# Kernel tuning notes

Measured on AMD Instinct MI355X. Metric: run time of the kernel, lower is better.

The kernel has to match this reference:

```python
import jax, jax.numpy as jnp
import numpy as np

B, D_IN, D_H = 16384, 512, 1024


def _glorot(key, out_d, in_d):
    lim = 1.0 / np.sqrt(in_d)
    return jax.random.uniform(key, (out_d, in_d), minval=-lim, maxval=lim, dtype=jnp.float32)


def setup_inputs() -> dict:
    key = jax.random.key(0)
    ks = jax.random.split(key, 16)
    inp = {
        "x_t": jax.random.normal(ks[0], (B, D_IN), dtype=jnp.float32),
        "delta_t": jax.random.uniform(ks[1], (B, 1), dtype=jnp.float32),
        "h_prev": jax.random.normal(ks[2], (B, D_H), dtype=jnp.float32),
        # torch nn.Linear weights are [out, in]; y = x @ W.T
        "W_sh": _glorot(ks[3], D_H, D_H),
        "W_sx": _glorot(ks[4], D_H, D_IN),
        "W_st": _glorot(ks[5], D_H, 1),
        "b_s": jnp.zeros((D_H,), jnp.float32),
        "WTh": _glorot(ks[6], D_H, D_H),
        "WTx": _glorot(ks[7], D_H, D_IN),
        "WTs": _glorot(ks[8], D_H, D_H),
        "b_T": jnp.zeros((D_H,), jnp.float32),
        "W_rh": _glorot(ks[9], D_H, D_H),
        "W_rx": _glorot(ks[10], D_H, D_IN),
        "b_r": jnp.zeros((D_H,), jnp.float32),
        "W_zh": _glorot(ks[11], D_H, D_H),
        "W_zx": _glorot(ks[12], D_H, D_IN),
        "b_z": jnp.zeros((D_H,), jnp.float32),
        "W_h": _glorot(ks[13], D_H, D_H),
        "W_x": _glorot(ks[14], D_H, D_IN),
        "b": jnp.zeros((D_H,), jnp.float32),
    }
    return inp


def reference(x_t, delta_t, h_prev,
              W_sh, W_sx, W_st, b_s,
              WTh, WTx, WTs, b_T,
              W_rh, W_rx, b_r,
              W_zh, W_zx, b_z,
              W_h, W_x, b):
    lin = lambda x, W: x @ W.T  # nn.Linear(bias=False)
    s_t = jnp.tanh(lin(h_prev, W_sh) + lin(x_t, W_sx) + lin(delta_t, W_st) + b_s)
    T_t = jax.nn.sigmoid(lin(h_prev, WTh) + lin(x_t, WTx) + lin(s_t, WTs) + b_T)
    r_t = jax.nn.sigmoid(lin(h_prev, W_rh) + lin(x_t, W_rx) + b_r)
    z_t = jax.nn.sigmoid(lin(h_prev, W_zh) + lin(x_t, W_zx) + b_z)
    h_tilde = jnp.tanh(lin(r_t * h_prev, W_h) + lin(x_t, W_x) + b)
    h_t = (1.0 - z_t) * (T_t * h_prev) + z_t * h_tilde
    return h_t
```

## Files before the change

### kernel.cpp

```cpp
#include <hip/hip_runtime.h>
#include <stdint.h>

#define AS1 __attribute__((address_space(1)))
#define AS3 __attribute__((address_space(3)))

typedef unsigned short US;
typedef __bf16 bf16x8 __attribute__((ext_vector_type(8)));
typedef float f32x4 __attribute__((ext_vector_type(4)));

static constexpr int Bsz = 16384;
static constexpr int DIN = 512;
static constexpr int DH  = 1024;
static constexpr int LDA = 2560;
static constexpr int LDR = 1536;

__device__ __forceinline__ US f2bf(float f) {
  unsigned u = __float_as_uint(f);
  u += 0x7fffu + ((u >> 16) & 1u);
  return (US)(u >> 16);
}
__device__ __forceinline__ float bf2f(US u) { return __uint_as_float(((unsigned)u) << 16); }
__device__ __forceinline__ float sigm(float x) { return 1.f / (1.f + __expf(-x)); }
__device__ __forceinline__ float tanh_f(float x) { return 1.f - 2.f / (1.f + __expf(2.f * x)); }

__global__ void pack_A(const float* __restrict__ h, const float* __restrict__ x,
                       US* __restrict__ Ab, US* __restrict__ RHx) {
  const int total = Bsz * 384;
  for (int idx = blockIdx.x * blockDim.x + threadIdx.x; idx < total;
       idx += gridDim.x * blockDim.x) {
    int row = idx / 384;
    int c = (idx - row * 384) * 4;
    const float* src = (c < DH) ? (h + (size_t)row * DH + c)
                                : (x + (size_t)row * DIN + (c - DH));
    float4 v = *(const float4*)src;
    ushort4 o;
    o.x = f2bf(v.x); o.y = f2bf(v.y); o.z = f2bf(v.z); o.w = f2bf(v.w);
    *(ushort4*)(Ab + (size_t)row * LDA + c) = o;
    if (c >= DH) *(ushort4*)(RHx + (size_t)row * LDR + c) = o;
  }
}

struct WSlot { const float* src; US* dst; int n4; int ksh; int ld; int co; };
struct WBatch { WSlot s[11]; };
__global__ void conv_w(WBatch b) {
  WSlot sl = b.s[blockIdx.y];
  const int mask = (1 << sl.ksh) - 1;
  for (int i = blockIdx.x * blockDim.x + threadIdx.x; i < sl.n4;
       i += gridDim.x * blockDim.x) {
    float4 v = *(const float4*)(sl.src + (size_t)i * 4);
    ushort4 o;
    o.x = f2bf(v.x); o.y = f2bf(v.y); o.z = f2bf(v.z); o.w = f2bf(v.w);
    int r = i >> sl.ksh;
    int cc = (i & mask) * 4;
    *(ushort4*)(sl.dst + (size_t)r * sl.ld + sl.co + cc) = o;
  }
}

template <int EPI>
__global__ __launch_bounds__(512, 2) void gemm8(
    const US* __restrict__ A, int lda,
    const US* __restrict__ W, int ldw, int nt,
    const float* __restrict__ bias,
    const void* aux0, const void* aux1, const void* aux2,
    void* outp, int ldo) {
  __shared__ __align__(16) US As[2][256 * 64];
  __shared__ __align__(16) US Bs[2][256 * 64];

  const int tid  = threadIdx.x;
  const int lane = tid & 63;
  const int w    = tid >> 6;
  const int wr   = w >> 2;
  const int wc   = w & 3;
  const int quad = lane >> 4, l15 = lane & 15;
  const int sw8  = l15 & 7;
  const int lrow = lane >> 3;
  const int scc  = (lane & 7) ^ (lrow & 7);

  const int p = blockIdx.x;
  const int c = p & 7, q = p >> 3;
  const int nIdx = q & 3, mIdx = c * 8 + (q >> 2);
  const int mBase = mIdx * 256, nBase = nIdx * 256;

  f32x4 acc[8][4];
#pragma unroll
  for (int i = 0; i < 8; i++)
#pragma unroll
    for (int j = 0; j < 4; j++) acc[i][j] = f32x4{0.f, 0.f, 0.f, 0.f};

#define STAGE_A(d, hh, tt)                                                       \
  { const US* g = A + (size_t)(mBase + (hh)*128 + w * 8 + lrow) * lda +          \
                  (tt) * 64 + scc * 8;                                           \
    __builtin_amdgcn_global_load_lds((AS1 const void*)g,                         \
        (AS3 void*)&As[d][((hh)*128 + w * 8) * 64], 16, 0, 0);                   \
    __builtin_amdgcn_global_load_lds((AS1 const void*)(g + (size_t)64 * lda),    \
        (AS3 void*)&As[d][((hh)*128 + 64 + w * 8) * 64], 16, 0, 0); }
#define STAGE_B(d, hh, tt)                                                       \
  { const US* g = W + (size_t)(nBase + (hh)*128 + w * 8 + lrow) * ldw +          \
                  (tt) * 64 + scc * 8;                                           \
    __builtin_amdgcn_global_load_lds((AS1 const void*)g,                         \
        (AS3 void*)&Bs[d][((hh)*128 + w * 8) * 64], 16, 0, 0);                   \
    __builtin_amdgcn_global_load_lds((AS1 const void*)(g + (size_t)64 * ldw),    \
        (AS3 void*)&Bs[d][((hh)*128 + 64 + w * 8) * 64], 16, 0, 0); }

#define READ_A(mh)                                                               \
  _Pragma("unroll")                                                              \
  for (int i = 0; i < 4; ++i)                                                    \
    _Pragma("unroll")                                                            \
    for (int ks = 0; ks < 2; ++ks)                                               \
      af[i][ks] = *(const bf16x8*)&As[cur][(wr * 128 + (mh)*64 + i * 16 + l15)   \
                                          * 64 + (((ks * 4 + quad) ^ sw8) * 8)];
#define READ_B(BSET, nh)                                                         \
  _Pragma("unroll")                                                              \
  for (int j = 0; j < 2; ++j)                                                    \
    _Pragma("unroll")                                                            \
    for (int ks = 0; ks < 2; ++ks)                                               \
      BSET[j][ks] = *(const bf16x8*)&Bs[cur][(wc * 64 + (nh)*32 + j * 16 + l15)  \
                                            * 64 + (((ks * 4 + quad) ^ sw8) * 8)];
#define MFMA_Q(mh, BSET, nh)                                                     \
  _Pragma("unroll")                                                              \
  for (int ks = 0; ks < 2; ++ks)                                                 \
    _Pragma("unroll")                                                            \
    for (int i = 0; i < 4; ++i)                                                  \
      _Pragma("unroll")                                                          \
      for (int j = 0; j < 2; ++j)                                                \
        acc[(mh)*4 + i][(nh)*2 + j] = __builtin_amdgcn_mfma_f32_16x16x32_bf16(   \
            af[i][ks], BSET[j][ks], acc[(mh)*4 + i][(nh)*2 + j], 0, 0, 0);

  STAGE_A(0, 0, 0); STAGE_A(0, 1, 0); STAGE_B(0, 0, 0); STAGE_B(0, 1, 0);
  if (nt > 1) { STAGE_B(1, 0, 1); STAGE_B(1, 1, 1); }
  if (nt > 1) __builtin_amdgcn_s_waitcnt(0x0f74);
  else        __builtin_amdgcn_s_waitcnt(0x0f70);
  __builtin_amdgcn_s_barrier();
  __builtin_amdgcn_sched_barrier(0);

  bf16x8 af[4][2], b0[2][2], b1[2][2];
  int cur = 0;

  for (int t = 0; t < nt; ++t, cur ^= 1) {
    const int nxt = cur ^ 1;
    READ_A(0);
    READ_B(b0, 0);
    if (t + 1 < nt) STAGE_A(nxt, 0, t + 1);
    __builtin_amdgcn_s_barrier();
    __builtin_amdgcn_s_setprio(1);
    MFMA_Q(0, b0, 0);
    __builtin_amdgcn_s_setprio(0);
    __builtin_amdgcn_s_barrier();
    READ_B(b1, 1);
    if (t + 1 < nt) STAGE_A(nxt, 1, t + 1);
    __builtin_amdgcn_s_barrier();
    __builtin_amdgcn_s_setprio(1);
    MFMA_Q(0, b1, 1);
    __builtin_amdgcn_s_setprio(0);
    __builtin_amdgcn_s_barrier();
    READ_A(1);
    if (t + 2 < nt) STAGE_B(cur, 0, t + 2);
    __builtin_amdgcn_s_barrier();
    __builtin_amdgcn_s_setprio(1);
    MFMA_Q(1, b0, 0);
    __builtin_amdgcn_s_setprio(0);
    __builtin_amdgcn_s_barrier();
    if (t + 2 < nt) STAGE_B(cur, 1, t + 2);
    __builtin_amdgcn_s_barrier();
    __builtin_amdgcn_s_setprio(1);
    MFMA_Q(1, b1, 1);
    __builtin_amdgcn_s_setprio(0);
    if (t + 1 < nt) {
      if (t + 2 < nt) __builtin_amdgcn_s_waitcnt(0x0f74);
      else            __builtin_amdgcn_s_waitcnt(0x0f70);
      __builtin_amdgcn_s_barrier();
      __builtin_amdgcn_sched_barrier(0);
    }
  }
#undef STAGE_A
#undef STAGE_B
#undef READ_A
#undef READ_B
#undef MFMA_Q

#pragma unroll
  for (int im = 0; im < 8; ++im) {
#pragma unroll
    for (int jn = 0; jn < 4; ++jn) {
      const int col = nBase + wc * 64 + jn * 16 + l15;
      const float bv = bias[col];
#pragma unroll
      for (int r = 0; r < 4; ++r) {
        const int row = mBase + wr * 128 + im * 16 + quad * 4 + r;
        float v = acc[im][jn][r] + bv;
        if constexpr (EPI == 0) {
          const float* delta = (const float*)aux0;
          const float* wst   = (const float*)aux1;
          v += delta[row] * wst[col];
          ((US*)outp)[(size_t)row * ldo + col] = f2bf(tanh_f(v));
        } else if constexpr (EPI == 1) {
          const float* hp = (const float*)aux0;
          float rr = sigm(v);
          ((US*)outp)[(size_t)row * ldo + col] =
              f2bf(rr * hp[(size_t)row * DH + col]);
        } else if constexpr (EPI == 2) {
          ((US*)outp)[(size_t)row * ldo + col] = f2bf(sigm(v));
        } else if constexpr (EPI == 3) {
          ((US*)outp)[(size_t)row * ldo + col] = f2bf(tanh_f(v));
        } else {
          const float* hp = (const float*)aux0;
          const US* Zp = (const US*)aux1;
          const US* Hp = (const US*)aux2;
          float T = sigm(v);
          size_t o = (size_t)row * DH + col;
          float z = bf2f(Zp[o]), ht = bf2f(Hp[(size_t)row * LDR + col]);
          float h = hp[o];
          ((float*)outp)[(size_t)row * ldo + col] = (1.f - z) * (T * h) + z * ht;
        }
      }
    }
  }
}

extern "C" void kernel_launch(void* const* d_in, const int* in_sizes, int n_in,
                              void* d_out, int out_size, void* d_ws, size_t ws_size,
                              hipStream_t stream) {
  const float* x_t   = (const float*)d_in[0];
  const float* delta = (const float*)d_in[1];
  const float* h_prev= (const float*)d_in[2];
  const float* W_sh  = (const float*)d_in[3];
  const float* W_sx  = (const float*)d_in[4];
  const float* W_st  = (const float*)d_in[5];
  const float* b_s   = (const float*)d_in[6];
  const float* WTh   = (const float*)d_in[7];
  const float* WTx   = (const float*)d_in[8];
  const float* WTs   = (const float*)d_in[9];
  const float* b_T   = (const float*)d_in[10];
  const float* W_rh  = (const float*)d_in[11];
  const float* W_rx  = (const float*)d_in[12];
  const float* b_r   = (const float*)d_in[13];
  const float* W_zh  = (const float*)d_in[14];
  const float* W_zx  = (const float*)d_in[15];
  const float* b_z   = (const float*)d_in[16];
  const float* W_h   = (const float*)d_in[17];
  const float* W_x   = (const float*)d_in[18];
  const float* b_    = (const float*)d_in[19];
  float* out = (float*)d_out;

  char* ws = (char*)d_ws;
  US* Ab = (US*)ws;                         size_t off = (size_t)Bsz * LDA * 2;
  US* RH = (US*)(ws + off);                 off += (size_t)Bsz * LDR * 2;
  US* Zb = (US*)(ws + off);                 off += (size_t)Bsz * DH * 2;
  US* bWs = (US*)(ws + off); off += (size_t)DH * 1536 * 2;
  US* bWr = (US*)(ws + off); off += (size_t)DH * 1536 * 2;
  US* bWz = (US*)(ws + off); off += (size_t)DH * 1536 * 2;
  US* bWT = (US*)(ws + off); off += (size_t)DH * 2560 * 2;
  US* bWh = (US*)(ws + off); off += (size_t)DH * 1536 * 2;

  pack_A<<<dim3(8192), 256, 0, stream>>>(h_prev, x_t, Ab, RH);
  WBatch wb;
  const int n4h = DH * DH / 4, n4x = DH * DIN / 4;
  wb.s[0]  = {W_sh, bWs, n4h, 8, 1536, 0};
  wb.s[1]  = {W_sx, bWs, n4x, 7, 1536, 1024};
  wb.s[2]  = {W_rh, bWr, n4h, 8, 1536, 0};
  wb.s[3]  = {W_rx, bWr, n4x, 7, 1536, 1024};
  wb.s[4]  = {W_zh, bWz, n4h, 8, 1536, 0};
  wb.s[5]  = {W_zx, bWz, n4x, 7, 1536, 1024};
  wb.s[6]  = {WTh,  bWT, n4h, 8, 2560, 0};
  wb.s[7]  = {WTx,  bWT, n4x, 7, 2560, 1024};
  wb.s[8]  = {WTs,  bWT, n4h, 8, 2560, 1536};
  wb.s[9]  = {W_h,  bWh, n4h, 8, 1536, 0};
  wb.s[10] = {W_x,  bWh, n4x, 7, 1536, 1024};
  conv_w<<<dim3(512, 11), 256, 0, stream>>>(wb);

  const dim3 grid(256);

  gemm8<0><<<grid, 512, 0, stream>>>(Ab, LDA, bWs, 1536, 24, b_s,
                                     delta, W_st, nullptr, (void*)(Ab + 1536), LDA);
  gemm8<1><<<grid, 512, 0, stream>>>(Ab, LDA, bWr, 1536, 24, b_r,
                                     h_prev, nullptr, nullptr, (void*)RH, LDR);
  gemm8<2><<<grid, 512, 0, stream>>>(Ab, LDA, bWz, 1536, 24, b_z,
                                     nullptr, nullptr, nullptr, (void*)Zb, DH);
  gemm8<3><<<grid, 512, 0, stream>>>(RH, LDR, bWh, 1536, 24, b_,
                                     nullptr, nullptr, nullptr, (void*)RH, LDR);
  gemm8<4><<<grid, 512, 0, stream>>>(Ab, LDA, bWT, 2560, 40, b_T,
                                     h_prev, Zb, RH, (void*)out, DH);
}
```

Baseline: 577.1 us.

## Fuse s/r/z gate GEMMs into one launch and deepen LDS prefetch pipeline

Concatenates the s, r and z weight matrices into one 3072-row weight buffer and computes all three gates in a single GEMM launch with 768 blocks, picking the epilogue per N-block group. The main loop now prefetches both A and B two k-tiles ahead, issues LDS reads as inline ds_read_b128 with explicit lgkmcnt waits and sched barriers, and waits on vmcnt(8). h_tilde is written to a separate buffer instead of overwriting RH. The aim is fewer launches, a larger grid to fill the GPU, and better overlap of global loads with MFMA, at the cost of extra workspace and hand-managed waits that are fragile.

```diff
diff --git a/kernel.cpp b/kernel.cpp
--- a/kernel.cpp
+++ b/kernel.cpp
@@ -7,6 +7,7 @@
 typedef unsigned short US;
 typedef __bf16 bf16x8 __attribute__((ext_vector_type(8)));
 typedef float f32x4 __attribute__((ext_vector_type(4)));
+typedef int intx4 __attribute__((ext_vector_type(4)));
 
 static constexpr int Bsz = 16384;
 static constexpr int DIN = 512;
@@ -22,6 +23,16 @@
 __device__ __forceinline__ float bf2f(US u) { return __uint_as_float(((unsigned)u) << 16); }
 __device__ __forceinline__ float sigm(float x) { return 1.f / (1.f + __expf(-x)); }
 __device__ __forceinline__ float tanh_f(float x) { return 1.f - 2.f / (1.f + __expf(2.f * x)); }
+
+__device__ __forceinline__ intx4 dsr128(unsigned addr) {
+  intx4 r;
+  asm volatile("ds_read_b128 %0, %1" : "=v"(r) : "v"(addr));
+  return r;
+}
+
+#define SBAR  asm volatile("s_barrier")
+#define SB0   __builtin_amdgcn_sched_barrier(0)
+#define LGKM0 { asm volatile("s_waitcnt lgkmcnt(0)"); __builtin_amdgcn_sched_barrier(0); }
 
 __global__ void pack_A(const float* __restrict__ h, const float* __restrict__ x,
                        US* __restrict__ Ab, US* __restrict__ RHx) {
@@ -56,13 +67,14 @@
   }
 }
 
-template <int EPI>
+template <int EPI, int NBLK>
 __global__ __launch_bounds__(512, 2) void gemm8(
     const US* __restrict__ A, int lda,
     const US* __restrict__ W, int ldw, int nt,
-    const float* __restrict__ bias,
+    const float* __restrict__ bias0, const float* __restrict__ bias1,
+    const float* __restrict__ bias2,
     const void* aux0, const void* aux1, const void* aux2,
-    void* outp, int ldo) {
+    void* out0, int ldo0, void* out1, void* out2) {
   __shared__ __align__(16) US As[2][256 * 64];
   __shared__ __align__(16) US Bs[2][256 * 64];
 
@@ -78,7 +90,7 @@
 
   const int p = blockIdx.x;
   const int c = p & 7, q = p >> 3;
-  const int nIdx = q & 3, mIdx = c * 8 + (q >> 2);
+  const int nIdx = q % NBLK, mIdx = c * 8 + q / NBLK;
   const int mBase = mIdx * 256, nBase = nIdx * 256;
 
   f32x4 acc[8][4];
@@ -87,16 +99,24 @@
 #pragma unroll
     for (int j = 0; j < 4; j++) acc[i][j] = f32x4{0.f, 0.f, 0.f, 0.f};
 
-#define STAGE_A(d, hh, tt)                                                       \
-  { const US* g = A + (size_t)(mBase + (hh)*128 + w * 8 + lrow) * lda +          \
-                  (tt) * 64 + scc * 8;                                           \
+  const unsigned aBase = (unsigned)(uintptr_t)&As[0][0];
+  const unsigned bBase = (unsigned)(uintptr_t)&Bs[0][0];
+  const unsigned arB = (unsigned)((wr * 128 + l15) * 128);
+  const unsigned brB = (unsigned)((wc * 64 + l15) * 128);
+  const unsigned kc0 = (unsigned)((quad ^ sw8) * 16);
+
+  const size_t aRowS = (size_t)(mBase + w * 8 + lrow) * lda;
+  const size_t wRowS = (size_t)(nBase + w * 8 + lrow) * ldw;
+  const int sccOff = scc * 8;
+
+#define STAGE_A(d, hh, co)                                                       \
+  { const US* g = A + aRowS + (size_t)(hh) * 128 * lda + (co) + sccOff;          \
     __builtin_amdgcn_global_load_lds((AS1 const void*)g,                         \
         (AS3 void*)&As[d][((hh)*128 + w * 8) * 64], 16, 0, 0);                   \
     __builtin_amdgcn_global_load_lds((AS1 const void*)(g + (size_t)64 * lda),    \
         (AS3 void*)&As[d][((hh)*128 + 64 + w * 8) * 64], 16, 0, 0); }
-#define STAGE_B(d, hh, tt)                                                       \
-  { const US* g = W + (size_t)(nBase + (hh)*128 + w * 8 + lrow) * ldw +          \
-                  (tt) * 64 + scc * 8;                                           \
+#define STAGE_B(d, hh, co)                                                       \
+  { const US* g = W + wRowS + (size_t)(hh) * 128 * ldw + (co) + sccOff;          \
     __builtin_amdgcn_global_load_lds((AS1 const void*)g,                         \
         (AS3 void*)&Bs[d][((hh)*128 + w * 8) * 64], 16, 0, 0);                   \
     __builtin_amdgcn_global_load_lds((AS1 const void*)(g + (size_t)64 * ldw),    \
@@ -107,15 +127,15 @@
   for (int i = 0; i < 4; ++i)                                                    \
     _Pragma("unroll")                                                            \
     for (int ks = 0; ks < 2; ++ks)                                               \
-      af[i][ks] = *(const bf16x8*)&As[cur][(wr * 128 + (mh)*64 + i * 16 + l15)   \
-                                          * 64 + (((ks * 4 + quad) ^ sw8) * 8)];
+      af[i][ks] = dsr128(aC + arB + (mh)*8192u + (unsigned)i * 2048u +           \
+                         (kc0 ^ (unsigned)(ks << 6)));
 #define READ_B(BSET, nh)                                                         \
   _Pragma("unroll")                                                              \
   for (int j = 0; j < 2; ++j)                                                    \
     _Pragma("unroll")                                                            \
     for (int ks = 0; ks < 2; ++ks)                                               \
-      BSET[j][ks] = *(const bf16x8*)&Bs[cur][(wc * 64 + (nh)*32 + j * 16 + l15)  \
-                                            * 64 + (((ks * 4 + quad) ^ sw8) * 8)];
+      BSET[j][ks] = dsr128(bC + brB + (nh)*4096u + (unsigned)j * 2048u +         \
+                           (kc0 ^ (unsigned)(ks << 6)));
 #define MFMA_Q(mh, BSET, nh)                                                     \
   _Pragma("unroll")                                                              \
   for (int ks = 0; ks < 2; ++ks)                                                 \
@@ -124,52 +144,55 @@
       _Pragma("unroll")                                                          \
       for (int j = 0; j < 2; ++j)                                                \
         acc[(mh)*4 + i][(nh)*2 + j] = __builtin_amdgcn_mfma_f32_16x16x32_bf16(   \
-            af[i][ks], BSET[j][ks], acc[(mh)*4 + i][(nh)*2 + j], 0, 0, 0);
-
-  STAGE_A(0, 0, 0); STAGE_A(0, 1, 0); STAGE_B(0, 0, 0); STAGE_B(0, 1, 0);
-  if (nt > 1) { STAGE_B(1, 0, 1); STAGE_B(1, 1, 1); }
-  if (nt > 1) __builtin_amdgcn_s_waitcnt(0x0f74);
-  else        __builtin_amdgcn_s_waitcnt(0x0f70);
-  __builtin_amdgcn_s_barrier();
-  __builtin_amdgcn_sched_barrier(0);
-
-  bf16x8 af[4][2], b0[2][2], b1[2][2];
+            __builtin_bit_cast(bf16x8, af[i][ks]),                               \
+            __builtin_bit_cast(bf16x8, BSET[j][ks]),                             \
+            acc[(mh)*4 + i][(nh)*2 + j], 0, 0, 0);
+
+  STAGE_B(0, 0, 0); STAGE_B(0, 1, 0); STAGE_A(0, 0, 0); STAGE_A(0, 1, 0);
+  STAGE_B(1, 0, 64); STAGE_B(1, 1, 64); STAGE_A(1, 0, 64); STAGE_A(1, 1, 64);
+  asm volatile("s_waitcnt vmcnt(8)");
+  SBAR; SB0;
+
+  intx4 af[4][2], b0[2][2], b1[2][2];
   int cur = 0;
 
   for (int t = 0; t < nt; ++t, cur ^= 1) {
-    const int nxt = cur ^ 1;
+    const unsigned aC = aBase + (unsigned)cur * 32768u;
+    const unsigned bC = bBase + (unsigned)cur * 32768u;
+    const bool haveS = (t + 2 < nt);
+    const int co2 = (t + 2) * 64;
     READ_A(0);
     READ_B(b0, 0);
-    if (t + 1 < nt) STAGE_A(nxt, 0, t + 1);
-    __builtin_amdgcn_s_barrier();
+    SBAR; SB0;
+    LGKM0;
     __builtin_amdgcn_s_setprio(1);
     MFMA_Q(0, b0, 0);
     __builtin_amdgcn_s_setprio(0);
-    __builtin_amdgcn_s_barrier();
+    SBAR; SB0;
     READ_B(b1, 1);
-    if (t + 1 < nt) STAGE_A(nxt, 1, t + 1);
-    __builtin_amdgcn_s_barrier();
+    SBAR; SB0;
+    LGKM0;
     __builtin_amdgcn_s_setprio(1);
     MFMA_Q(0, b1, 1);
     __builtin_amdgcn_s_setprio(0);
-    __builtin_amdgcn_s_barrier();
+    SBAR; SB0;
     READ_A(1);
-    if (t + 2 < nt) STAGE_B(cur, 0, t + 2);
-    __builtin_amdgcn_s_barrier();
+    if (haveS) { STAGE_B(cur, 0, co2); STAGE_B(cur, 1, co2); }
+    SBAR; SB0;
+    LGKM0;
     __builtin_amdgcn_s_setprio(1);
     MFMA_Q(1, b0, 0);
     __builtin_amdgcn_s_setprio(0);
-    __builtin_amdgcn_s_barrier();
-    if (t + 2 < nt) STAGE_B(cur, 1, t + 2);
-    __builtin_amdgcn_s_barrier();
+    SBAR; SB0;
+    if (haveS) { STAGE_A(cur, 0, co2); STAGE_A(cur, 1, co2); }
+    SBAR; SB0;
     __builtin_amdgcn_s_setprio(1);
     MFMA_Q(1, b1, 1);
     __builtin_amdgcn_s_setprio(0);
     if (t + 1 < nt) {
-      if (t + 2 < nt) __builtin_amdgcn_s_waitcnt(0x0f74);
-      else            __builtin_amdgcn_s_waitcnt(0x0f70);
-      __builtin_amdgcn_s_barrier();
-      __builtin_amdgcn_sched_barrier(0);
+      if (haveS) { asm volatile("s_waitcnt vmcnt(8)"); }
+      else       { asm volatile("s_waitcnt vmcnt(0)"); }
+      SBAR; SB0;
     }
   }
 #undef STAGE_A
@@ -183,34 +206,51 @@
 #pragma unroll
     for (int jn = 0; jn < 4; ++jn) {
       const int col = nBase + wc * 64 + jn * 16 + l15;
-      const float bv = bias[col];
-#pragma unroll
-      for (int r = 0; r < 4; ++r) {
-        const int row = mBase + wr * 128 + im * 16 + quad * 4 + r;
-        float v = acc[im][jn][r] + bv;
-        if constexpr (EPI == 0) {
-          const float* delta = (const float*)aux0;
-          const float* wst   = (const float*)aux1;
-          v += delta[row] * wst[col];
-          ((US*)outp)[(size_t)row * ldo + col] = f2bf(tanh_f(v));
-        } else if constexpr (EPI == 1) {
-          const float* hp = (const float*)aux0;
-          float rr = sigm(v);
-          ((US*)outp)[(size_t)row * ldo + col] =
-              f2bf(rr * hp[(size_t)row * DH + col]);
-        } else if constexpr (EPI == 2) {
-          ((US*)outp)[(size_t)row * ldo + col] = f2bf(sigm(v));
-        } else if constexpr (EPI == 3) {
-          ((US*)outp)[(size_t)row * ldo + col] = f2bf(tanh_f(v));
-        } else {
-          const float* hp = (const float*)aux0;
-          const US* Zp = (const US*)aux1;
-          const US* Hp = (const US*)aux2;
+      if constexpr (EPI == 0) {
+        const int g = nIdx >> 2;
+        const int colg = col & 1023;
+        const float* bp = (g == 0) ? bias0 : (g == 1) ? bias1 : bias2;
+        const float bv = bp[colg];
+        const float* delta = (const float*)aux0;
+        const float* wst   = (const float*)aux1;
+        const float* hp    = (const float*)aux2;
+#pragma unroll
+        for (int r = 0; r < 4; ++r) {
+          const int row = mBase + wr * 128 + im * 16 + quad * 4 + r;
+          float v = acc[im][jn][r] + bv;
+          if (g == 0) {
+            v += delta[row] * wst[colg];
+            ((US*)out0)[(size_t)row * ldo0 + colg] = f2bf(tanh_f(v));
+          } else if (g == 1) {
+            float rr = sigm(v);
+            ((US*)out1)[(size_t)row * LDR + colg] =
+                f2bf(rr * hp[(size_t)row * DH + colg]);
+          } else {
+            ((US*)out2)[(size_t)row * DH + colg] = f2bf(sigm(v));
+          }
+        }
+      } else if constexpr (EPI == 3) {
+        const float bv = bias0[col];
+#pragma unroll
+        for (int r = 0; r < 4; ++r) {
+          const int row = mBase + wr * 128 + im * 16 + quad * 4 + r;
+          float v = acc[im][jn][r] + bv;
+          ((US*)out0)[(size_t)row * ldo0 + col] = f2bf(tanh_f(v));
+        }
+      } else {
+        const float bv = bias0[col];
+        const float* hp = (const float*)aux0;
+        const US* Zp = (const US*)aux1;
+        const US* Hp = (const US*)aux2;
+#pragma unroll
+        for (int r = 0; r < 4; ++r) {
+          const int row = mBase + wr * 128 + im * 16 + quad * 4 + r;
+          float v = acc[im][jn][r] + bv;
           float T = sigm(v);
           size_t o = (size_t)row * DH + col;
-          float z = bf2f(Zp[o]), ht = bf2f(Hp[(size_t)row * LDR + col]);
+          float z = bf2f(Zp[o]), ht = bf2f(Hp[o]);
           float h = hp[o];
-          ((float*)outp)[(size_t)row * ldo + col] = (1.f - z) * (T * h) + z * ht;
+          ((float*)out0)[(size_t)row * ldo0 + col] = (1.f - z) * (T * h) + z * ht;
         }
       }
     }
@@ -243,41 +283,39 @@
   float* out = (float*)d_out;
 
   char* ws = (char*)d_ws;
-  US* Ab = (US*)ws;                         size_t off = (size_t)Bsz * LDA * 2;
-  US* RH = (US*)(ws + off);                 off += (size_t)Bsz * LDR * 2;
-  US* Zb = (US*)(ws + off);                 off += (size_t)Bsz * DH * 2;
-  US* bWs = (US*)(ws + off); off += (size_t)DH * 1536 * 2;
-  US* bWr = (US*)(ws + off); off += (size_t)DH * 1536 * 2;
-  US* bWz = (US*)(ws + off); off += (size_t)DH * 1536 * 2;
-  US* bWT = (US*)(ws + off); off += (size_t)DH * 2560 * 2;
-  US* bWh = (US*)(ws + off); off += (size_t)DH * 1536 * 2;
+  US* Ab  = (US*)ws;              size_t off = (size_t)Bsz * LDA * 2;
+  US* RH  = (US*)(ws + off);      off += (size_t)Bsz * LDR * 2;
+  US* Zb  = (US*)(ws + off);      off += (size_t)Bsz * DH * 2;
+  US* HTb = (US*)(ws + off);      off += (size_t)Bsz * DH * 2;
+  US* bWsrz = (US*)(ws + off);    off += (size_t)3072 * 1536 * 2;
+  US* bWT   = (US*)(ws + off);    off += (size_t)DH * 2560 * 2;
+  US* bWh   = (US*)(ws + off);    off += (size_t)DH * 1536 * 2;
 
   pack_A<<<dim3(8192), 256, 0, stream>>>(h_prev, x_t, Ab, RH);
   WBatch wb;
   const int n4h = DH * DH / 4, n4x = DH * DIN / 4;
-  wb.s[0]  = {W_sh, bWs, n4h, 8, 1536, 0};
-  wb.s[1]  = {W_sx, bWs, n4x, 7, 1536, 1024};
-  wb.s[2]  = {W_rh, bWr, n4h, 8, 1536, 0};
-  wb.s[3]  = {W_rx, bWr, n4x, 7, 1536, 1024};
-  wb.s[4]  = {W_zh, bWz, n4h, 8, 1536, 0};
-  wb.s[5]  = {W_zx, bWz, n4x, 7, 1536, 1024};
-  wb.s[6]  = {WTh,  bWT, n4h, 8, 2560, 0};
-  wb.s[7]  = {WTx,  bWT, n4x, 7, 2560, 1024};
-  wb.s[8]  = {WTs,  bWT, n4h, 8, 2560, 1536};
-  wb.s[9]  = {W_h,  bWh, n4h, 8, 1536, 0};
-  wb.s[10] = {W_x,  bWh, n4x, 7, 1536, 1024};
+  US* bWr = bWsrz + (size_t)1024 * 1536;
+  US* bWz = bWsrz + (size_t)2048 * 1536;
+  wb.s[0]  = {W_sh, bWsrz, n4h, 8, 1536, 0};
+  wb.s[1]  = {W_sx, bWsrz, n4x, 7, 1536, 1024};
+  wb.s[2]  = {W_rh, bWr,   n4h, 8, 1536, 0};
+  wb.s[3]  = {W_rx, bWr,   n4x, 7, 1536, 1024};
+  wb.s[4]  = {W_zh, bWz,   n4h, 8, 1536, 0};
+  wb.s[5]  = {W_zx, bWz,   n4x, 7, 1536, 1024};
+  wb.s[6]  = {WTh,  bWT,   n4h, 8, 2560, 0};
+  wb.s[7]  = {WTx,  bWT,   n4x, 7, 2560, 1024};
+  wb.s[8]  = {WTs,  bWT,   n4h, 8, 2560, 1536};
+  wb.s[9]  = {W_h,  bWh,   n4h, 8, 1536, 0};
+  wb.s[10] = {W_x,  bWh,   n4x, 7, 1536, 1024};
   conv_w<<<dim3(512, 11), 256, 0, stream>>>(wb);
 
-  const dim3 grid(256);
-
-  gemm8<0><<<grid, 512, 0, stream>>>(Ab, LDA, bWs, 1536, 24, b_s,
-                                     delta, W_st, nullptr, (void*)(Ab + 1536), LDA);
-  gemm8<1><<<grid, 512, 0, stream>>>(Ab, LDA, bWr, 1536, 24, b_r,
-                                     h_prev, nullptr, nullptr, (void*)RH, LDR);
-  gemm8<2><<<grid, 512, 0, stream>>>(Ab, LDA, bWz, 1536, 24, b_z,
-                                     nullptr, nullptr, nullptr, (void*)Zb, DH);
-  gemm8<3><<<grid, 512, 0, stream>>>(RH, LDR, bWh, 1536, 24, b_,
-                                     nullptr, nullptr, nullptr, (void*)RH, LDR);
-  gemm8<4><<<grid, 512, 0, stream>>>(Ab, LDA, bWT, 2560, 40, b_T,
-                                     h_prev, Zb, RH, (void*)out, DH);
-}
+  gemm8<0, 12><<<dim3(768), 512, 0, stream>>>(
+      Ab, LDA, bWsrz, 1536, 24, b_s, b_r, b_z,
+      delta, W_st, h_prev, (void*)(Ab + 1536), LDA, (void*)RH, (void*)Zb);
+  gemm8<3, 4><<<dim3(256), 512, 0, stream>>>(
+      RH, LDR, bWh, 1536, 24, b_, nullptr, nullptr,
+      nullptr, nullptr, nullptr, (void*)HTb, DH, nullptr, nullptr);
+  gemm8<4, 4><<<dim3(256), 512, 0, stream>>>(
+      Ab, LDA, bWT, 2560, 40, b_T, nullptr, nullptr,
+      h_prev, Zb, HTb, (void*)out, DH, nullptr, nullptr);
+}
```

Result: slower. 688.9 us (+19.4%).
